# Optimization experiments

Hardware: AMD Instinct MI355X
Metric: run time of the kernel (lower is better)

Reference implementation:

```python
import jax, jax.numpy as jnp
import numpy as np
import math

B, S, D = 4, 2048, 1024
H, HD, L = 16, 64, 512
ROPE_BASE = 10000.0
EPS = 1e-6


def _rope_angles(seq_len, head_dim, base):
    # (seq_len, head_dim//2) rotation angles
    inv_freq = 1.0 / (base ** (jnp.arange(0, head_dim, 2, dtype=jnp.float32) / head_dim))
    pos = jnp.arange(seq_len, dtype=jnp.float32)
    return pos[:, None] * inv_freq[None, :]


def _apply_rope(t, ang):
    # t: (B, H, S, HD); half-split rotation (rotate-half convention)
    cos = jnp.cos(ang)  # (S, HD//2)
    sin = jnp.sin(ang)
    t1, t2 = jnp.split(t, 2, axis=-1)
    return jnp.concatenate([t1 * cos - t2 * sin, t1 * sin + t2 * cos], axis=-1)


def setup_inputs() -> dict:
    key = jax.random.key(0)
    ks = jax.random.split(key, 7)
    def w(k, shape, fan_in):
        return jax.random.normal(k, shape, jnp.float32) * (fan_in ** -0.5)
    return {
        "x": jax.random.normal(ks[0], (B, S, D), jnp.float32),
        "norm_w": jnp.ones((D,), jnp.float32),
        "wq": w(ks[1], (D, H * HD), D),
        "kv_down": w(ks[2], (D, L), D),
        "wk": w(ks[3], (L, H * HD), L),
        "wv": w(ks[4], (L, H * HD), L),
        "wo": w(ks[5], (H * HD, D), H * HD),
    }


def reference(x, norm_w, wq, kv_down, wk, wv, wo):
    residual = x
    # RMSNorm
    var = jnp.mean(x * x, axis=-1, keepdims=True)
    xn = x * jax.lax.rsqrt(var + EPS) * norm_w
    # Projections: q from full x, k/v from latent down-projection
    q = (xn @ wq).reshape(B, S, H, HD).transpose(0, 2, 1, 3)          # (B,H,S,HD)
    kv = xn @ kv_down                                                  # (B,S,L)
    k = (kv @ wk).reshape(B, S, H, HD).transpose(0, 2, 1, 3)
    v = (kv @ wv).reshape(B, S, H, HD).transpose(0, 2, 1, 3)
    # RoPE
    ang = _rope_angles(S, HD, ROPE_BASE)
    q = _apply_rope(q, ang)
    k = _apply_rope(k, ang)
    # Attention (full, no mask)
    scale = 1.0 / math.sqrt(HD)
    attn = jnp.einsum("bhsd,bhtd->bhst", q, k) * scale
    attn = jax.nn.softmax(attn, axis=-1)
    out = jnp.einsum("bhst,bhtd->bhsd", attn, v)
    out = out.transpose(0, 2, 1, 3).reshape(B, S, H * HD) @ wo
    return residual + out
```

## Files before the change

### kernel.cpp

```cpp
#include <hip/hip_runtime.h>

typedef unsigned short u16;
typedef unsigned int   u32;
typedef __attribute__((ext_vector_type(8)))  __bf16 bf16x8;
typedef __attribute__((ext_vector_type(2)))  __bf16 bf16x2;
typedef __attribute__((ext_vector_type(8)))  short  short8;
typedef __attribute__((ext_vector_type(4)))  float  f32x4;
typedef __attribute__((ext_vector_type(16))) float  f32x16;
typedef __attribute__((ext_vector_type(4)))  u16    u16x4;
typedef __attribute__((ext_vector_type(4)))  u32    u32x4;

#define DEV static __device__ __forceinline__

DEV u16 f2bf(float f){ return __builtin_bit_cast(u16, (__bf16)f); }
DEV u32 pkbf(float a, float b){ bf16x2 t; t[0] = (__bf16)a; t[1] = (__bf16)b;
                                return __builtin_bit_cast(u32, t); }

#if __has_builtin(__builtin_amdgcn_exp2f)
DEV float fexp2(float x){ return __builtin_amdgcn_exp2f(x); }
#else
DEV float fexp2(float x){ return exp2f(x); }
#endif

DEV f32x4 mfma16(short8 a, short8 b, f32x4 c){
  return __builtin_amdgcn_mfma_f32_16x16x32_bf16(
      __builtin_bit_cast(bf16x8, a), __builtin_bit_cast(bf16x8, b), c, 0, 0, 0);
}
DEV f32x16 mfma32(short8 a, short8 b, f32x16 c){
  return __builtin_amdgcn_mfma_f32_32x32x16_bf16(
      __builtin_bit_cast(bf16x8, a), __builtin_bit_cast(bf16x8, b), c, 0, 0, 0);
}
DEV int swz(int byteoff, int row){ return byteoff ^ ((row & 7) << 4); }

#if __has_builtin(__builtin_amdgcn_global_load_lds)
#define USE_GLL 1
typedef __attribute__((address_space(1))) const u32 gas_u32;
typedef __attribute__((address_space(3)))       u32 las_u32;
#define GL2L(g, l) __builtin_amdgcn_global_load_lds((gas_u32*)(g), (las_u32*)(l), 16, 0, 0)
#endif

template<int N> DEV void wbar(){
  if constexpr (N == 4)
    asm volatile("s_waitcnt vmcnt(4) lgkmcnt(0)\ns_barrier" ::: "memory");
  else if constexpr (N == 3)
    asm volatile("s_waitcnt vmcnt(3) lgkmcnt(0)\ns_barrier" ::: "memory");
  else
    asm volatile("s_waitcnt vmcnt(0) lgkmcnt(0)\ns_barrier" ::: "memory");
  __builtin_amdgcn_sched_barrier(0);
}

__global__ __launch_bounds__(256) void k_prep(const float* __restrict__ wq,
                                              const float* __restrict__ kvd,
                                              const float* __restrict__ wk,
                                              const float* __restrict__ wv,
                                              const float* __restrict__ wo,
                                              const float* __restrict__ x,
                                              const float* __restrict__ norm_w,
                                              u16* __restrict__ wqT, u16* __restrict__ kvdT,
                                              u16* __restrict__ wkT, u16* __restrict__ wvT,
                                              u16* __restrict__ woT, u16* __restrict__ xn,
                                              float2* __restrict__ cs, float qscale){
  const int z = blockIdx.z;
  if (z == 6){
    const int bid = blockIdx.y*32 + blockIdx.x;
    const int t = threadIdx.x;
    __shared__ float ps[4];
    const float4 g = ((const float4*)norm_w)[t];
    #pragma unroll 1
    for (int it = 0; it < 8; ++it){
      const int row = bid*8 + it;
      const float4 v = ((const float4*)(x + (size_t)row*1024))[t];
      float ss = v.x*v.x + v.y*v.y + v.z*v.z + v.w*v.w;
      #pragma unroll
      for (int off=32; off; off>>=1) ss += __shfl_xor(ss, off, 64);
      if ((t & 63) == 0) ps[t>>6] = ss;
      __syncthreads();
      const float tot = ps[0]+ps[1]+ps[2]+ps[3];
      const float rinv = rsqrtf(tot * (1.0f/1024.0f) + 1e-6f);
      u16x4 o;
      o.x = f2bf(v.x*rinv*g.x); o.y = f2bf(v.y*rinv*g.y);
      o.z = f2bf(v.z*rinv*g.z); o.w = f2bf(v.w*rinv*g.w);
      *(u16x4*)(xn + (size_t)row*1024 + t*4) = o;
      __syncthreads();
    }
    return;
  }
  if (z == 5){
    if (blockIdx.y >= 8) return;
    const int idx = (blockIdx.y*32 + blockIdx.x)*256 + threadIdx.x;
    const int s = idx >> 5, j = idx & 31;
    const float ang = (float)s * expf(-(float)j * (9.210340371976184f/32.0f));
    cs[idx] = make_float2(cosf(ang), sinf(ang));
    return;
  }
  const float* W; u16* Wt; int K, N; float sc = 1.0f;
  switch (z){
    case 0: W = wq;  Wt = wqT;  K = 1024; N = 1024; sc = qscale; break;
    case 1: W = kvd; Wt = kvdT; K = 1024; N = 512;  break;
    case 2: W = wk;  Wt = wkT;  K = 512;  N = 1024; break;
    case 3: W = wv;  Wt = wvT;  K = 512;  N = 1024; break;
    default: W = wo; Wt = woT;  K = 1024; N = 1024; break;
  }
  const int k0 = blockIdx.x*32, n0 = blockIdx.y*32;
  if (k0 >= K || n0 >= N) return;
  __shared__ float t[32][33];
  const int tx = threadIdx.x & 31, ty = threadIdx.x >> 5;
  #pragma unroll
  for (int j=0;j<4;++j) t[ty + j*8][tx] = W[(size_t)(k0+ty+j*8)*N + n0 + tx];
  __syncthreads();
  #pragma unroll
  for (int j=0;j<4;++j) Wt[(size_t)(n0+ty+j*8)*K + k0 + tx] = f2bf(t[tx][ty+j*8]*sc);
}

template<int MODE, int BM>
__global__ __launch_bounds__(512, 2) void k_gemm8(const u16* __restrict__ A,
                                                  const u16* __restrict__ Bt,
                                                  const u16* __restrict__ Bt2,
                                                  u16* __restrict__ Cb,
                                                  u16* __restrict__ Cb2,
                                                  float* __restrict__ Cf,
                                                  const float* __restrict__ resid,
                                                  const float2* __restrict__ cs,
                                                  int K){
  constexpr int MFR   = BM/32;
  constexpr int ASZ   = BM*64;
  constexpr int BSZ   = 16384;
  constexpr int HALFB = 2*ASZ + 2*BSZ;
  constexpr int AGLL  = BM/128;
  constexpr int LPH   = AGLL + 2;
  __shared__ __align__(16) char Lds[2*HALFB];

  const int tid = threadIdx.x, lane = tid & 63, w = tid >> 6;
  const int lr = lane & 15, lg = lane >> 4;
  const int wm = (w >> 2)*(BM/2), wn = (w & 3)*64;

  const int gx = gridDim.x;
  const int nwg = gx * gridDim.y;
  int fid = blockIdx.y*gx + blockIdx.x;
  fid = (fid & 7)*(nwg >> 3) + (fid >> 3);
  const int bx = fid % gx, by = fid / gx;

  const bool second = (MODE != 2) && (bx >= 4);
  const u16* Bp = second ? Bt2 : Bt;
  const int n0 = (second ? bx - 4 : bx)*256;
  const int m0 = by*BM;
  const int nt = K >> 6;

  f32x4 acc[MFR][4] = {};

  int aoff[MFR], boff[4];
  #pragma unroll
  for (int m=0;m<MFR;++m){ const int r = wm + m*16 + lr;
    aoff[m] = r*64 + ((lg ^ ((r>>1)&3)) << 4); }
  #pragma unroll
  for (int n=0;n<4;++n){ const int r = wn + n*16 + lr;
    boff[n] = r*64 + ((lg ^ ((r>>1)&3)) << 4); }

  const int rin = lane >> 2, sl = lane & 3;
  u32 Ago[AGLL], Bgo[2];
  int AdO[AGLL], BdO[2];
  #pragma unroll
  for (int i=0;i<AGLL;++i){
    const int br = (BM == 256) ? (w*32 + i*16) : (w*16);
    const int row = br + rin;
    Ago[i] = (u32)row*(u32)(K*2) + (u32)((sl ^ ((row>>1)&3)) << 4);
    AdO[i] = br*64;
  }
  #pragma unroll
  for (int i=0;i<2;++i){
    const int br = w*32 + i*16;
    const int row = br + rin;
    Bgo[i] = (u32)row*(u32)(K*2) + (u32)((sl ^ ((row>>1)&3)) << 4);
    BdO[i] = br*64;
  }
  const char* Abase = (const char*)(A  + (size_t)m0*K);
  const char* Bbase = (const char*)(Bp + (size_t)n0*K);

#ifdef USE_GLL
  #define ISSA(kh, t1, db) { _Pragma("unroll")                                   \
    for (int i_=0;i_<AGLL;++i_)                                                  \
      GL2L(Abase + (size_t)((t1)*128 + (kh)*64) + Ago[i_],                       \
           Lds + (db) + (kh)*ASZ + AdO[i_]); }
  #define ISSB(kh, t1, db) { _Pragma("unroll")                                   \
    for (int i_=0;i_<2;++i_)                                                     \
      GL2L(Bbase + (size_t)((t1)*128 + (kh)*64) + Bgo[i_],                       \
           Lds + (db) + 2*ASZ + (kh)*BSZ + BdO[i_]); }
#else
  #define ISSA(kh, t1, db) { _Pragma("unroll")                                   \
    for (int i_=0;i_<AGLL;++i_)                                                  \
      *(short8*)(Lds + (db) + (kh)*ASZ + AdO[i_] + lane*16) =                    \
        *(const short8*)(Abase + (size_t)((t1)*128 + (kh)*64) + Ago[i_]); }
  #define ISSB(kh, t1, db) { _Pragma("unroll")                                   \
    for (int i_=0;i_<2;++i_)                                                     \
      *(short8*)(Lds + (db) + 2*ASZ + (kh)*BSZ + BdO[i_] + lane*16) =            \
        *(const short8*)(Bbase + (size_t)((t1)*128 + (kh)*64) + Bgo[i_]); }
#endif

  #define CHALF(kh, bbv) {                                                       \
    short8 bfr_[4], af_[MFR];                                                    \
    _Pragma("unroll")                                                            \
    for (int n=0;n<4;++n)                                                        \
      bfr_[n] = *(const short8*)(Lds + (bbv) + 2*ASZ + (kh)*BSZ + boff[n]);      \
    _Pragma("unroll")                                                            \
    for (int m=0;m<MFR;++m)                                                      \
      af_[m] = *(const short8*)(Lds + (bbv) + (kh)*ASZ + aoff[m]);               \
    __builtin_amdgcn_s_setprio(1);                                               \
    _Pragma("unroll")                                                            \
    for (int m=0;m<MFR;++m)                                                      \
      _Pragma("unroll")                                                          \
      for (int n=0;n<4;++n)                                                      \
        acc[m][n] = mfma16(af_[m], bfr_[n], acc[m][n]);                          \
    __builtin_amdgcn_s_setprio(0); }

  u32 bb = 0;
  ISSA(0, 0, 0); ISSB(0, 0, 0); ISSA(1, 0, 0); ISSB(1, 0, 0);

  #pragma unroll 1
  for (int t = 0; t < nt-1; ++t){
    wbar<LPH>();
    ISSA(0, t+1, bb^HALFB); ISSB(0, t+1, bb^HALFB);
    CHALF(0, bb);
    wbar<LPH>();
    ISSA(1, t+1, bb^HALFB); ISSB(1, t+1, bb^HALFB);
    CHALF(1, bb);
    bb ^= HALFB;
  }
  wbar<LPH>();
  CHALF(0, bb);
  wbar<0>();
  CHALF(1, bb);

  #pragma unroll
  for (int m=0;m<MFR;++m){
    const int rb = m0 + wm + m*16 + lg*4;
    if (MODE == 2){
      #pragma unroll
      for (int n=0;n<4;++n){
        const int c = n0 + wn + n*16 + lr;
        #pragma unroll
        for (int i=0;i<4;++i){
          const size_t off = (size_t)(rb+i)*1024 + c;
          Cf[off] = acc[m][n][i] + resid[off];
        }
      }
    } else if (!second){
      #pragma unroll
      for (int n=0;n<2;++n){
        const int c = n0 + wn + n*16 + lr;
        const int j = n*16 + lr;
        #pragma unroll
        for (int i=0;i<4;++i){
          const float2 t = cs[(size_t)((rb+i) & 2047)*32 + j];
          const float t1 = acc[m][n][i], t2 = acc[m][n+2][i];
          Cb[(size_t)(rb+i)*1024 + c]      = f2bf(t1*t.x - t2*t.y);
          Cb[(size_t)(rb+i)*1024 + c + 32] = f2bf(t1*t.y + t2*t.x);
        }
      }
    } else if (MODE == 4){
      #pragma unroll
      for (int n=0;n<4;++n){
        const int c = n0 + wn + n*16 + lr;
        #pragma unroll
        for (int i=0;i<4;++i) Cb2[(size_t)(rb+i)*512 + c] = f2bf(acc[m][n][i]);
      }
    } else {
      #pragma unroll
      for (int n=0;n<4;++n){
        const int c = n0 + wn + n*16 + lr;
        const int b = rb >> 11, s = rb & 2047;
        u16x4 pk;
        pk.x = f2bf(acc[m][n][0]); pk.y = f2bf(acc[m][n][1]);
        pk.z = f2bf(acc[m][n][2]); pk.w = f2bf(acc[m][n][3]);
        *(u16x4*)(Cb2 + (((size_t)(b*1024 + c)) << 11) + s) = pk;
      }
    }
  }
  #undef ISSA
  #undef ISSB
  #undef CHALF
}

__global__ __launch_bounds__(512, 4) void k_attn(const u16* __restrict__ q,
                                                 const u16* __restrict__ kmat,
                                                 const u16* __restrict__ vT,
                                                 u16* __restrict__ o){
  __shared__ __align__(16) u16 Kl[2][64*64];
  __shared__ __align__(16) u16 Vl[2][64*64];
  const int tid = threadIdx.x, lane = tid & 63, w = tid >> 6;
  const int l31 = lane & 31, hi = lane >> 5;

  const int fid = blockIdx.y * 8 + blockIdx.x;
  const int sid = (fid & 7) * 64 + (fid >> 3);
  const int qx = sid & 7, bh = sid >> 3;
  const int b = bh >> 4, h = bh & 15;
  const int q0 = qx * 256;

  short8 qf[4];
  {
    const size_t base = ((size_t)(b*2048 + q0 + w*32 + l31) << 10) + (h<<6) + hi*8;
    qf[0] = *(const short8*)(q + base);
    qf[1] = *(const short8*)(q + base + 16);
    qf[2] = *(const short8*)(q + base + 32);
    qf[3] = *(const short8*)(q + base + 48);
  }
  f32x16 oacc0 = {}, oacc1 = {};
  f32x16 accl  = {};
  const short8 ones = {0x3F80,0x3F80,0x3F80,0x3F80,0x3F80,0x3F80,0x3F80,0x3F80};

  int roff[8];
  #pragma unroll
  for (int c=0;c<4;++c){
    roff[c*2+0] = swz(l31*128      + c*32 + hi*16, l31);
    roff[c*2+1] = swz((32+l31)*128 + c*32 + hi*16, 32+l31);
  }

  const int rin  = lane >> 3;
  const int colq = (lane & 7) ^ rin;
  const u16* kp0 = kmat + ((size_t)(b*2048 + w*8 + rin) << 10) + (h<<6) + colq*8;
  const u16* vp0 = vT + (((size_t)(b*1024 + h*64 + w*8 + rin)) << 11) + colq*8;
  u16* const Kd0 = Kl[0] + w*512;  u16* const Kd1 = Kl[1] + w*512;
  u16* const Vd0 = Vl[0] + w*512;  u16* const Vd1 = Vl[1] + w*512;

#ifdef USE_GLL
  #define STAGE(KD, VD) { GL2L(kp0, KD); GL2L(vp0, VD);                         \
      kp0 += 65536; vp0 += 64; }
#else
  #define STAGE(KD, VD) { *(short8*)(KD + lane*8) = *(const short8*)(kp0);      \
      *(short8*)(VD + lane*8) = *(const short8*)(vp0);                          \
      kp0 += 65536; vp0 += 64; }
#endif

  #define TILE(BOFF) {                                                          \
    f32x16 s0 = {}, s1 = {};                                                    \
    __builtin_amdgcn_s_setprio(1);                                              \
    _Pragma("unroll")                                                           \
    for (int c=0;c<4;++c){                                                      \
      short8 kf0 = *(const short8*)((const char*)Kl + roff[c*2+0] + BOFF);      \
      short8 kf1 = *(const short8*)((const char*)Kl + roff[c*2+1] + BOFF);      \
      s0 = mfma32(kf0, qf[c], s0);                                              \
      s1 = mfma32(kf1, qf[c], s1);                                              \
    }                                                                           \
    __builtin_amdgcn_s_setprio(0);                                              \
    u32 pk0[8], pk1[8];                                                         \
    _Pragma("unroll")                                                           \
    for (int a=0;a<4;++a){                                                      \
      _Pragma("unroll")                                                         \
      for (int e=0;e<2;++e){                                                    \
        pk0[a*2+e] = pkbf(fexp2(s0[a*4+e*2]), fexp2(s0[a*4+e*2+1]));            \
        pk1[a*2+e] = pkbf(fexp2(s1[a*4+e*2]), fexp2(s1[a*4+e*2+1]));            \
      }                                                                         \
    }                                                                           \
    __builtin_amdgcn_s_setprio(1);                                              \
    _Pragma("unroll")                                                           \
    for (int c=0;c<4;++c){                                                      \
      u32* pks = (c < 2) ? pk0 : pk1;                                           \
      const int cc = c & 1;                                                     \
      u32 a0 = pks[(2*cc)*2+0], b0 = pks[(2*cc+1)*2+0];                         \
      u32 a1 = pks[(2*cc)*2+1], b1 = pks[(2*cc+1)*2+1];                         \
      asm volatile("v_permlane32_swap_b32 %0, %1" : "+v"(a0), "+v"(b0));        \
      asm volatile("v_permlane32_swap_b32 %0, %1" : "+v"(a1), "+v"(b1));        \
      u32x4 pfv; pfv.x = a0; pfv.y = a1; pfv.z = b0; pfv.w = b1;                \
      const short8 pf = __builtin_bit_cast(short8, pfv);                        \
      short8 vf0 = *(const short8*)((const char*)Vl + roff[c*2+0] + BOFF);      \
      short8 vf1 = *(const short8*)((const char*)Vl + roff[c*2+1] + BOFF);      \
      oacc0 = mfma32(pf, vf0, oacc0);                                           \
      oacc1 = mfma32(pf, vf1, oacc1);                                           \
      accl  = mfma32(pf, ones, accl);                                           \
    }                                                                           \
    __builtin_amdgcn_s_setprio(0);                                              \
  }

  STAGE(Kd0, Vd0);
  #pragma unroll 1
  for (int tt = 0; tt < 16; ++tt){
    __syncthreads();
    STAGE(Kd1, Vd1);
    TILE(0);
    __syncthreads();
    if (tt < 15) STAGE(Kd0, Vd0);
    TILE(8192);
  }

  #pragma unroll
  for (int reg=0; reg<16; ++reg){
    const int cq = (reg&3) + 8*(reg>>2) + 4*hi;
    const float lv = 1.0f / accl[reg];
    const size_t rowbase = ((size_t)(b*2048 + q0 + w*32 + cq) << 10) + (h<<6);
    o[rowbase + l31]      = f2bf(oacc0[reg] * lv);
    o[rowbase + 32 + l31] = f2bf(oacc1[reg] * lv);
  }
  #undef STAGE
  #undef TILE
}

extern "C" void kernel_launch(void* const* d_in, const int* in_sizes, int n_in,
                              void* d_out, int out_size, void* d_ws, size_t ws_size,
                              hipStream_t stream){
  const float* x      = (const float*)d_in[0];
  const float* norm_w = (const float*)d_in[1];
  const float* wq     = (const float*)d_in[2];
  const float* kvd    = (const float*)d_in[3];
  const float* wk     = (const float*)d_in[4];
  const float* wv     = (const float*)d_in[5];
  const float* wo     = (const float*)d_in[6];
  float* out = (float*)d_out;

  char* ws = (char*)d_ws;
  const size_t SZ = (size_t)8192*1024*2;
  u16* xn   = (u16*)(ws);
  u16* q    = (u16*)(ws + SZ);
  u16* kmat = (u16*)(ws + 2*SZ);
  u16* vT   = (u16*)(ws + 3*SZ);
  u16* attn = (u16*)(ws + 4*SZ);
  u16* kv   = (u16*)(ws + 5*SZ);
  u16* wqT  = (u16*)(ws + 5*SZ + (size_t)8192*512*2);
  u16* kvdT = wqT  + 1024*1024;
  u16* wkT  = kvdT + 512*1024;
  u16* wvT  = wkT  + 1024*512;
  u16* woT  = wvT  + 1024*512;
  float2* cs = (float2*)(woT + 1024*1024);

  const float QSCALE = 0.125f * 1.4426950408889634f;

  k_prep<<<dim3(32,32,7), 256, 0, stream>>>(wq, kvd, wk, wv, wo, x, norm_w,
                                            wqT, kvdT, wkT, wvT, woT, xn, cs, QSCALE);

  k_gemm8<4,256><<<dim3(6,32), 512, 0, stream>>>(xn, wqT, kvdT, q, kv, nullptr, nullptr, cs, 1024);
  k_gemm8<5,256><<<dim3(8,32), 512, 0, stream>>>(kv, wkT, wvT, kmat, vT, nullptr, nullptr, cs, 512);

  k_attn<<<dim3(8,64), 512, 0, stream>>>(q, kmat, vT, attn);

  k_gemm8<2,128><<<dim3(4,64), 512, 0, stream>>>(attn, woT, nullptr, nullptr, nullptr, out, x, nullptr, 1024);
}
```

Before: 168.8 us.

## Rebalance projection GEMMs: compute kv first, then fuse Q/K/V into one launch

Moves the kv down-projection into its own small 256-thread GEMM with 128x128 tiles. The Q projection (from xn) and the K and V projections (from kv) now share a single launch using 256x128 tiles, selected by a segment index with per-segment K. The output projection also switches to 256x128 tiles with 8 waves. The aim is better CU balance and fewer serialized launches, since Q no longer waits behind the kv dependency chain. In exchange the fused launch has segments of unequal length (K=1024 vs 512), and the tiles per wave change.

```diff
diff --git a/kernel.cpp b/kernel.cpp
--- a/kernel.cpp
+++ b/kernel.cpp
@@ -112,27 +112,32 @@
   for (int j=0;j<4;++j) Wt[(size_t)(n0+ty+j*8)*K + k0 + tx] = f2bf(t[tx][ty+j*8]*sc);
 }
 
-template<int MODE, int BM>
-__global__ __launch_bounds__(512, 2) void k_gemm8(const u16* __restrict__ A,
-                                                  const u16* __restrict__ Bt,
-                                                  const u16* __restrict__ Bt2,
-                                                  u16* __restrict__ Cb,
-                                                  u16* __restrict__ Cb2,
-                                                  float* __restrict__ Cf,
-                                                  const float* __restrict__ resid,
-                                                  const float2* __restrict__ cs,
-                                                  int K){
-  constexpr int MFR   = BM/32;
-  constexpr int ASZ   = BM*64;
-  constexpr int BSZ   = 16384;
+template<int MODE>
+__global__ __launch_bounds__((MODE==0)?256:512, 2)
+void k_gemm8(const u16* __restrict__ A1,
+             const u16* __restrict__ A2,
+             const u16* __restrict__ Bt0,
+             const u16* __restrict__ Bt1,
+             const u16* __restrict__ Bt2,
+             u16* __restrict__ Cb0,
+             u16* __restrict__ Cb1,
+             u16* __restrict__ Cb2,
+             float* __restrict__ Cf,
+             const float* __restrict__ resid,
+             const float2* __restrict__ cs){
+  constexpr int NW   = (MODE==0) ? 4 : 8;
+  constexpr int BM   = (MODE==0) ? 128 : 256;
+  constexpr int ASZ  = BM*64;
+  constexpr int BSZ  = 128*64;
   constexpr int HALFB = 2*ASZ + 2*BSZ;
-  constexpr int AGLL  = BM/128;
-  constexpr int LPH   = AGLL + 2;
+  constexpr int AGLL = 2;
+  constexpr int BGLL = 8/NW;
+  constexpr int LPH  = AGLL + BGLL;
   __shared__ __align__(16) char Lds[2*HALFB];
 
   const int tid = threadIdx.x, lane = tid & 63, w = tid >> 6;
   const int lr = lane & 15, lg = lane >> 4;
-  const int wm = (w >> 2)*(BM/2), wn = (w & 3)*64;
+  const int wm = (w >> 1)*64, wn = (w & 1)*64;
 
   const int gx = gridDim.x;
   const int nwg = gx * gridDim.y;
@@ -140,40 +145,42 @@
   fid = (fid & 7)*(nwg >> 3) + (fid >> 3);
   const int bx = fid % gx, by = fid / gx;
 
-  const bool second = (MODE != 2) && (bx >= 4);
-  const u16* Bp = second ? Bt2 : Bt;
-  const int n0 = (second ? bx - 4 : bx)*256;
-  const int m0 = by*BM;
-  const int nt = K >> 6;
-
-  f32x4 acc[MFR][4] = {};
-
-  int aoff[MFR], boff[4];
-  #pragma unroll
-  for (int m=0;m<MFR;++m){ const int r = wm + m*16 + lr;
+  const int seg = (MODE==1) ? (bx >> 3) : 0;
+  const int n0  = (MODE==1) ? ((bx & 7)*128) : (bx*128);
+  const int m0  = by*BM;
+  const int K   = (MODE==1) ? (seg ? 512 : 1024) : 1024;
+  const int nt  = K >> 6;
+  const u16* Ap = (MODE==1) ? (seg ? A2 : A1) : A1;
+  const u16* Bp = (MODE==1) ? (seg==0 ? Bt0 : (seg==1 ? Bt1 : Bt2)) : Bt0;
+
+  f32x4 acc[4][4] = {};
+
+  int aoff[4], boff[4];
+  #pragma unroll
+  for (int m=0;m<4;++m){ const int r = wm + m*16 + lr;
     aoff[m] = r*64 + ((lg ^ ((r>>1)&3)) << 4); }
   #pragma unroll
   for (int n=0;n<4;++n){ const int r = wn + n*16 + lr;
     boff[n] = r*64 + ((lg ^ ((r>>1)&3)) << 4); }
 
   const int rin = lane >> 2, sl = lane & 3;
-  u32 Ago[AGLL], Bgo[2];
-  int AdO[AGLL], BdO[2];
+  u32 Ago[AGLL], Bgo[BGLL];
+  int AdO[AGLL], BdO[BGLL];
   #pragma unroll
   for (int i=0;i<AGLL;++i){
-    const int br = (BM == 256) ? (w*32 + i*16) : (w*16);
+    const int br = w*(16*AGLL) + i*16;
     const int row = br + rin;
     Ago[i] = (u32)row*(u32)(K*2) + (u32)((sl ^ ((row>>1)&3)) << 4);
     AdO[i] = br*64;
   }
   #pragma unroll
-  for (int i=0;i<2;++i){
-    const int br = w*32 + i*16;
+  for (int i=0;i<BGLL;++i){
+    const int br = w*(16*BGLL) + i*16;
     const int row = br + rin;
     Bgo[i] = (u32)row*(u32)(K*2) + (u32)((sl ^ ((row>>1)&3)) << 4);
     BdO[i] = br*64;
   }
-  const char* Abase = (const char*)(A  + (size_t)m0*K);
+  const char* Abase = (const char*)(Ap + (size_t)m0*K);
   const char* Bbase = (const char*)(Bp + (size_t)n0*K);
 
 #ifdef USE_GLL
@@ -182,7 +189,7 @@
       GL2L(Abase + (size_t)((t1)*128 + (kh)*64) + Ago[i_],                       \
            Lds + (db) + (kh)*ASZ + AdO[i_]); }
   #define ISSB(kh, t1, db) { _Pragma("unroll")                                   \
-    for (int i_=0;i_<2;++i_)                                                     \
+    for (int i_=0;i_<BGLL;++i_)                                                  \
       GL2L(Bbase + (size_t)((t1)*128 + (kh)*64) + Bgo[i_],                       \
            Lds + (db) + 2*ASZ + (kh)*BSZ + BdO[i_]); }
 #else
@@ -191,22 +198,22 @@
       *(short8*)(Lds + (db) + (kh)*ASZ + AdO[i_] + lane*16) =                    \
         *(const short8*)(Abase + (size_t)((t1)*128 + (kh)*64) + Ago[i_]); }
   #define ISSB(kh, t1, db) { _Pragma("unroll")                                   \
-    for (int i_=0;i_<2;++i_)                                                     \
+    for (int i_=0;i_<BGLL;++i_)                                                  \
       *(short8*)(Lds + (db) + 2*ASZ + (kh)*BSZ + BdO[i_] + lane*16) =            \
         *(const short8*)(Bbase + (size_t)((t1)*128 + (kh)*64) + Bgo[i_]); }
 #endif
 
   #define CHALF(kh, bbv) {                                                       \
-    short8 bfr_[4], af_[MFR];                                                    \
+    short8 bfr_[4], af_[4];                                                      \
     _Pragma("unroll")                                                            \
     for (int n=0;n<4;++n)                                                        \
       bfr_[n] = *(const short8*)(Lds + (bbv) + 2*ASZ + (kh)*BSZ + boff[n]);      \
     _Pragma("unroll")                                                            \
-    for (int m=0;m<MFR;++m)                                                      \
+    for (int m=0;m<4;++m)                                                        \
       af_[m] = *(const short8*)(Lds + (bbv) + (kh)*ASZ + aoff[m]);               \
     __builtin_amdgcn_s_setprio(1);                                               \
     _Pragma("unroll")                                                            \
-    for (int m=0;m<MFR;++m)                                                      \
+    for (int m=0;m<4;++m)                                                        \
       _Pragma("unroll")                                                          \
       for (int n=0;n<4;++n)                                                      \
         acc[m][n] = mfma16(af_[m], bfr_[n], acc[m][n]);                          \
@@ -231,7 +238,7 @@
   CHALF(1, bb);
 
   #pragma unroll
-  for (int m=0;m<MFR;++m){
+  for (int m=0;m<4;++m){
     const int rb = m0 + wm + m*16 + lg*4;
     if (MODE == 2){
       #pragma unroll
@@ -243,7 +250,15 @@
           Cf[off] = acc[m][n][i] + resid[off];
         }
       }
-    } else if (!second){
+    } else if (MODE == 0){
+      #pragma unroll
+      for (int n=0;n<4;++n){
+        const int c = n0 + wn + n*16 + lr;
+        #pragma unroll
+        for (int i=0;i<4;++i) Cb0[(size_t)(rb+i)*512 + c] = f2bf(acc[m][n][i]);
+      }
+    } else if (seg < 2){
+      u16* dst = seg ? Cb1 : Cb0;
       #pragma unroll
       for (int n=0;n<2;++n){
         const int c = n0 + wn + n*16 + lr;
@@ -252,16 +267,9 @@
         for (int i=0;i<4;++i){
           const float2 t = cs[(size_t)((rb+i) & 2047)*32 + j];
           const float t1 = acc[m][n][i], t2 = acc[m][n+2][i];
-          Cb[(size_t)(rb+i)*1024 + c]      = f2bf(t1*t.x - t2*t.y);
-          Cb[(size_t)(rb+i)*1024 + c + 32] = f2bf(t1*t.y + t2*t.x);
+          dst[(size_t)(rb+i)*1024 + c]      = f2bf(t1*t.x - t2*t.y);
+          dst[(size_t)(rb+i)*1024 + c + 32] = f2bf(t1*t.y + t2*t.x);
         }
-      }
-    } else if (MODE == 4){
-      #pragma unroll
-      for (int n=0;n<4;++n){
-        const int c = n0 + wn + n*16 + lr;
-        #pragma unroll
-        for (int i=0;i<4;++i) Cb2[(size_t)(rb+i)*512 + c] = f2bf(acc[m][n][i]);
       }
     } else {
       #pragma unroll
@@ -425,10 +433,13 @@
   k_prep<<<dim3(32,32,7), 256, 0, stream>>>(wq, kvd, wk, wv, wo, x, norm_w,
                                             wqT, kvdT, wkT, wvT, woT, xn, cs, QSCALE);
 
-  k_gemm8<4,256><<<dim3(6,32), 512, 0, stream>>>(xn, wqT, kvdT, q, kv, nullptr, nullptr, cs, 1024);
-  k_gemm8<5,256><<<dim3(8,32), 512, 0, stream>>>(kv, wkT, wvT, kmat, vT, nullptr, nullptr, cs, 512);
+  k_gemm8<0><<<dim3(4,64), 256, 0, stream>>>(xn, nullptr, kvdT, nullptr, nullptr,
+                                             kv, nullptr, nullptr, nullptr, nullptr, nullptr);
+  k_gemm8<1><<<dim3(24,32), 512, 0, stream>>>(xn, kv, wqT, wkT, wvT,
+                                              q, kmat, vT, nullptr, nullptr, cs);
 
   k_attn<<<dim3(8,64), 512, 0, stream>>>(q, kmat, vT, attn);
 
-  k_gemm8<2,128><<<dim3(4,64), 512, 0, stream>>>(attn, woT, nullptr, nullptr, nullptr, out, x, nullptr, 1024);
-}
+  k_gemm8<2><<<dim3(8,32), 512, 0, stream>>>(attn, nullptr, woT, nullptr, nullptr,
+                                             nullptr, nullptr, nullptr, out, x, nullptr);
+}
```

Measured after the change: 170.8 us. No clear change (+1.2%).
